# Optimization experiments

Hardware: AMD Instinct MI355X
Metric: run time of the kernel (lower is better)

Reference implementation:

```python
import jax, jax.numpy as jnp
import numpy as np

# Tree config: batch of perfect binary trees in heap layout (root=0, children of i are 2i+1, 2i+2)
D_MODEL = 512
DEPTH = 10                      # number of internal levels
B = 64                          # number of trees in the batch
VOCAB = 32000
N_LEAVES = 2 ** DEPTH           # 1024 leaves per tree
N_NODES = 2 ** (DEPTH + 1) - 1  # 2047 nodes per tree
N_CLASSES = 2                   # binary graph classification


def setup_inputs() -> dict:
    key = jax.random.key(0)
    k_tok, k_emb, k_iou, k_f, k_out = jax.random.split(key, 5)
    d = D_MODEL
    s_in = 1.0 / np.sqrt(2 * d)
    return {
        "tokens": jax.random.randint(k_tok, (B, N_LEAVES), 0, VOCAB, dtype=jnp.int32),
        "embedding": (jax.random.normal(k_emb, (VOCAB, d), jnp.float32) * 0.02),
        "W_iou": jax.random.normal(k_iou, (2 * d, 3 * d), jnp.float32) * s_in,
        "b_iou": jnp.zeros((3 * d,), jnp.float32),
        "W_f": jax.random.normal(k_f, (2 * d, 2 * d), jnp.float32) * s_in,
        "b_f": jnp.zeros((2 * d,), jnp.float32),
        "W_out": jax.random.normal(k_out, (d, N_CLASSES), jnp.float32) * (1.0 / np.sqrt(d)),
    }


def reference(tokens, embedding, W_iou, b_iou, W_f, b_f, W_out):
    # Shared activation / memory buffers over all nodes, as in RecursiveNN.forward.
    d = embedding.shape[1]
    b = tokens.shape[0]
    h = jnp.zeros((b, N_NODES, d), jnp.float32)   # activations
    c = jnp.zeros((b, N_NODES, d), jnp.float32)   # memory (memory_size=1)

    # Leaves: embedding lookup, scattered into the activation buffer.
    leaf_h = embedding[tokens]                    # [B, N_LEAVES, d]
    h = h.at[:, N_LEAVES - 1:].set(leaf_h)

    # Internal nodes by topological level (leaf-adjacent level first, root last).
    for level in range(DEPTH - 1, -1, -1):
        idx = np.arange(2 ** level - 1, 2 ** (level + 1) - 1)  # node group (static)
        left, right = 2 * idx + 1, 2 * idx + 2                 # predecessor indices
        # Gather predecessor activations and memory.
        hl, hr = h[:, left], h[:, right]                       # [B, n, d]
        cl, cr = c[:, left], c[:, right]
        x = jnp.concatenate([hl, hr], axis=-1)                 # [B, n, 2d]
        # Binary TreeLSTM cell (the _apply_function for the 'add' binary op).
        iou = x @ W_iou + b_iou
        i, o, u = jnp.split(iou, 3, axis=-1)
        f = jax.nn.sigmoid(x @ W_f + b_f)
        fl, fr = jnp.split(f, 2, axis=-1)
        c_new = jax.nn.sigmoid(i) * jnp.tanh(u) + fl * cl + fr * cr
        h_new = jax.nn.sigmoid(o) * jnp.tanh(c_new)
        # Scatter back into the shared buffers.
        h = h.at[:, idx].set(h_new)
        c = c.at[:, idx].set(c_new)

    # _compute_output: linear binary-classification head on the root activation.
    return h[:, 0] @ W_out                                     # [B, N_CLASSES]
```

## Files before the change

### kernel.cpp

```cpp
#include <hip/hip_runtime.h>
#include <math.h>

typedef unsigned short u16;
typedef short s16x8 __attribute__((ext_vector_type(8)));
typedef float f32x4 __attribute__((ext_vector_type(4)));

#define NITER 32
#define ARW 72

__device__ __align__(16) u16 g_Bhi[1024 * 2560];
__device__ __align__(16) u16 g_Blo[1024 * 2560];
__device__ __align__(16) u16 g_Aleaf[(size_t)64 * 1024 * 1024];

__device__ __forceinline__ u16 f2bf(float x) {
    unsigned u = __float_as_uint(x);
    u += 0x7fffu + ((u >> 16) & 1u);
    return (u16)(u >> 16);
}
__device__ __forceinline__ float bf2f(u16 h) { return __uint_as_float(((unsigned)h) << 16); }
__device__ __forceinline__ float sigm(float x) { return 1.0f / (1.0f + expf(-x)); }
__device__ __forceinline__ unsigned pk(u16 a, u16 b) { return (unsigned)a | ((unsigned)b << 16); }

__device__ __forceinline__ void gload16(const void* g, u16* l) {
    __builtin_amdgcn_global_load_lds(
        (const __attribute__((address_space(1))) void*)g,
        (__attribute__((address_space(3))) void*)(void*)l, 16, 0, 0);
}

__global__ __launch_bounds__(256)
void wsplit_kernel(const float* __restrict__ Wiou, const float* __restrict__ Wf)
{
    __shared__ float tile[32][65];
    const int kb = blockIdx.x;
    const int cb = blockIdx.y;
    const int t  = threadIdx.x;
    const int c0 = cb * 64;

    {
        const int kk  = t >> 3;
        const int cu0 = (t & 7) * 8;
        const int k   = kb * 32 + kk;
#pragma unroll
        for (int u = 0; u < 8; u++) {
            int c = c0 + cu0 + u;
            float v = (c < 1536) ? Wiou[(size_t)k * 1536 + c]
                                 : Wf[(size_t)k * 1024 + (c - 1536)];
            tile[kk][cu0 + u] = v;
        }
    }
    __syncthreads();
    {
        const int jl = t >> 2;
        const int kc = (t & 3) * 8;
        const int g  = c0 >> 9;
        const int j  = (c0 & 511) + jl;
        size_t dst = (((size_t)kb * 5 + g) * 512 + j) * 32 + kc;
        unsigned ph[4], pl[4];
#pragma unroll
        for (int u = 0; u < 4; u++) {
            float v0 = tile[kc + 2 * u][jl];
            float v1 = tile[kc + 2 * u + 1][jl];
            u16 h0 = f2bf(v0), h1 = f2bf(v1);
            u16 l0 = f2bf(v0 - bf2f(h0)), l1 = f2bf(v1 - bf2f(h1));
            ph[u] = pk(h0, h1);
            pl[u] = pk(l0, l1);
        }
        *(uint4*)(g_Bhi + dst) = make_uint4(ph[0], ph[1], ph[2], ph[3]);
        *(uint4*)(g_Blo + dst) = make_uint4(pl[0], pl[1], pl[2], pl[3]);
    }
}

__global__ __launch_bounds__(256)
void leafgather_kernel(const int* __restrict__ tokens, const float* __restrict__ emb)
{
    const int gidx = blockIdx.x * 256 + threadIdx.x;
    const int row  = gidx >> 5;
    const int c    = gidx & 31;
    const int tok  = tokens[row];
    const float* src = emb + (size_t)tok * 512 + c * 16;
    u16* dst = g_Aleaf + (size_t)row * 1024 + c * 32;

    float4 f0 = *(const float4*)(src);
    float4 f1 = *(const float4*)(src + 4);
    float4 f2 = *(const float4*)(src + 8);
    float4 f3 = *(const float4*)(src + 12);
    float v[16] = {f0.x,f0.y,f0.z,f0.w, f1.x,f1.y,f1.z,f1.w,
                   f2.x,f2.y,f2.z,f2.w, f3.x,f3.y,f3.z,f3.w};
    unsigned ph[8], pl[8];
#pragma unroll
    for (int i = 0; i < 8; i++) {
        u16 h0 = f2bf(v[2*i]),   h1 = f2bf(v[2*i+1]);
        u16 l0 = f2bf(v[2*i]   - bf2f(h0));
        u16 l1 = f2bf(v[2*i+1] - bf2f(h1));
        ph[i] = pk(h0, h1);
        pl[i] = pk(l0, l1);
    }
    *(uint4*)(dst)      = make_uint4(ph[0], ph[1], ph[2], ph[3]);
    *(uint4*)(dst + 8)  = make_uint4(ph[4], ph[5], ph[6], ph[7]);
    *(uint4*)(dst + 16) = make_uint4(pl[0], pl[1], pl[2], pl[3]);
    *(uint4*)(dst + 24) = make_uint4(pl[4], pl[5], pl[6], pl[7]);
}

template<bool LEAF>
__global__ __launch_bounds__(256, 2)
void level_big(const u16* __restrict__ Hcin, const float* __restrict__ Cc,
               const float* __restrict__ b_iou, const float* __restrict__ b_f,
               u16* __restrict__ Hp, float* __restrict__ Cp,
               int np, int lgnp)
{
    __shared__ __align__(16) u16 Ab0[8192];
    __shared__ __align__(16) u16 Ab1[8192];

    const u16* Hc = LEAF ? g_Aleaf : Hcin;

    const int tid = threadIdx.x;
    const int jg  = blockIdx.x;
    const int m0  = blockIdx.y * 64;
    const int j0  = jg * 64;
    const int nc  = np * 2;

    const int w    = tid >> 6;
    const int lane = tid & 63;
    const int il   = lane & 15;
    const int kq   = lane >> 4;
    const int wc   = w;

    f32x4 acc[4][5];
#pragma unroll
    for (int rf = 0; rf < 4; rf++)
#pragma unroll
        for (int g = 0; g < 5; g++) acc[rf][g] = (f32x4)0.0f;

    const int bA  = m0 >> lgnp;
    const int pA0 = m0 & (np - 1);
    const char* A0u = (const char*)(Hc + ((size_t)bA * nc + 2 * pA0) * 1024);
    const int rowS = tid >> 3;
    const int segS = (tid & 7) ^ (rowS & 7);
    const unsigned voffA = (unsigned)rowS * 4096u + (unsigned)segS * 16u;

    const int shi = ((kq >> 1) << 2) | (kq & 1);
    const int x7  = il & 7;
    const int aoh = il * 64 + ((shi ^ x7) * 8);
    const int aol = il * 64 + (((shi + 2) ^ x7) * 8);

    const char* BH0 = (const char*)(g_Bhi + (size_t)j0 * 32);
    const char* BL0 = (const char*)(g_Blo + (size_t)j0 * 32);
    unsigned vB[5];
#pragma unroll
    for (int g = 0; g < 5; g++)
        vB[g] = (unsigned)(((wc * 16 + il) * 32 + kq * 8) * 2 + g * 32768);

    s16x8 bh[5], bl[5];
    s16x8 ah[4], al[4];

#define STAGEA2(DST, t_)                                                       \
    {                                                                          \
        const char* ab = A0u + (size_t)(t_) * 128;                             \
        gload16(ab + voffA, (DST) + w * 512);                                  \
        gload16(ab + 131072 + voffA, (DST) + 2048 + w * 512);                  \
    }

#define LOADB_HI(t_)                                                           \
    {                                                                          \
        const char* bhp = BH0 + (size_t)(t_) * 163840;                         \
        _Pragma("unroll")                                                      \
        for (int g = 0; g < 5; g++) bh[g] = *(const s16x8*)(bhp + vB[g]);      \
    }

#define LOADB_LO(t_)                                                           \
    {                                                                          \
        const char* blp = BL0 + (size_t)(t_) * 163840;                         \
        _Pragma("unroll")                                                      \
        for (int g = 0; g < 5; g++) bl[g] = *(const s16x8*)(blp + vB[g]);      \
    }

#define READ_AH(ABASE)                                                         \
    {                                                                          \
        _Pragma("unroll")                                                      \
        for (int rf = 0; rf < 4; rf++)                                         \
            ah[rf] = *(const s16x8*)&(ABASE)[aoh + rf * 1024];                 \
    }

#define READ_AL(ABASE)                                                         \
    {                                                                          \
        _Pragma("unroll")                                                      \
        for (int rf = 0; rf < 4; rf++)                                         \
            al[rf] = *(const s16x8*)&(ABASE)[aol + rf * 1024];                 \
    }

#define MFMA_PASS(AREGS, BSET)                                                 \
    {                                                                          \
        __builtin_amdgcn_s_setprio(1);                                         \
        _Pragma("unroll")                                                      \
        for (int rf = 0; rf < 4; rf++)                                         \
            _Pragma("unroll")                                                  \
            for (int g = 0; g < 5; g++)                                        \
                acc[rf][g] = __builtin_amdgcn_mfma_f32_16x16x32_bf16(AREGS[rf], BSET[g], acc[rf][g], 0, 0, 0); \
        __builtin_amdgcn_s_setprio(0);                                         \
    }

#define WINDOW(ACUR, ANXT, t0_, more_)                                         \
    {                                                                          \
        if (more_) {                                                           \
            STAGEA2(ANXT, (t0_) + 2);                                          \
            STAGEA2((ANXT) + 4096, (t0_) + 3);                                 \
            __builtin_amdgcn_sched_barrier(0);                                 \
        }                                                                      \
                                    \
        MFMA_PASS(ah, bh);                                                     \
        MFMA_PASS(al, bh);                                \
        LOADB_HI((t0_) + 1);                                                   \
        READ_AL((ACUR) + 4096);                     \
        MFMA_PASS(ah, bl);                                \
        LOADB_LO((t0_) + 1);                                                   \
        READ_AH((ACUR) + 4096);                     \
                                         \
        MFMA_PASS(al, bh);                                                     \
        MFMA_PASS(ah, bh);                                        \
        if (more_) LOADB_HI((t0_) + 2);                                        \
        MFMA_PASS(ah, bl);                                        \
        if (more_) LOADB_LO((t0_) + 2);                                        \
        if (more_) {                                                           \
            asm volatile("s_waitcnt vmcnt(10)" ::: "memory");                  \
            __builtin_amdgcn_s_barrier();                                      \
            __builtin_amdgcn_sched_barrier(0);                                 \
            READ_AH(ANXT);                           \
            READ_AL(ANXT);                                                     \
        }                                                                      \
    }

    STAGEA2(Ab0, 0);
    STAGEA2(Ab0 + 4096, 1);
    __builtin_amdgcn_sched_barrier(0);
    LOADB_HI(0);
    LOADB_LO(0);
    asm volatile("s_waitcnt vmcnt(10)" ::: "memory");
    __builtin_amdgcn_s_barrier();
    __builtin_amdgcn_sched_barrier(0);
    READ_AH(Ab0);
    READ_AL(Ab0);

#pragma unroll 1
    for (int t0 = 0; t0 < NITER; t0 += 4) {
        WINDOW(Ab0, Ab1, t0, 1);
        WINDOW(Ab1, Ab0, t0 + 2, (t0 + 4 < NITER));
    }
#undef STAGEA2
#undef LOADB_HI
#undef LOADB_LO
#undef READ_AH
#undef READ_AL
#undef MFMA_PASS
#undef WINDOW

    const int jglob = j0 + wc * 16 + il;
    const float bi  = b_iou[jglob];
    const float bo_ = b_iou[512 + jglob];
    const float bu  = b_iou[1024 + jglob];
    const float bfl = b_f[jglob];
    const float bfr = b_f[512 + jglob];

#pragma unroll
    for (int rf = 0; rf < 4; rf++) {
#pragma unroll
        for (int r = 0; r < 4; r++) {
            const int m  = m0 + rf * 16 + kq * 4 + r;
            const int b  = m >> lgnp;
            const int p  = m & (np - 1);
            float i_ = acc[rf][0][r] + bi;
            float o_ = acc[rf][1][r] + bo_;
            float u_ = acc[rf][2][r] + bu;
            float fl = sigm(acc[rf][3][r] + bfl);
            float fr = sigm(acc[rf][4][r] + bfr);
            float cl = 0.0f, cr_ = 0.0f;
            if (!LEAF) {
                size_t cb_ = ((size_t)b * nc + 2 * p) * 512 + jglob;
                cl  = Cc[cb_];
                cr_ = Cc[cb_ + 512];
            }
            float cn = sigm(i_) * tanhf(u_) + fl * cl + fr * cr_;
            float hn = sigm(o_) * tanhf(cn);
            size_t prow = (size_t)b * np + p;
            u16 hh  = f2bf(hn);
            u16 hlo = f2bf(hn - bf2f(hh));
            Hp[prow * 1024 + (size_t)(jg * 4 + wc) * 32 + il]      = hh;
            Hp[prow * 1024 + (size_t)(jg * 4 + wc) * 32 + 16 + il] = hlo;
            Cp[prow * 512 + jglob] = cn;
        }
    }
}

__global__ __launch_bounds__(256, 2)
void level_small(const u16* __restrict__ Hc, const float* __restrict__ Cc,
                 const float* __restrict__ b_iou, const float* __restrict__ b_f,
                 u16* __restrict__ Hp, float* __restrict__ Cp,
                 int np, int lgnp)
{
    __shared__ __align__(16) u16 Ac[2][64 * ARW];

    const int tid = threadIdx.x;
    const int jg  = blockIdx.x;
    const int m0  = blockIdx.y * 64;
    const int j0  = jg * 64;
    const int nc  = np * 2;
    const int M   = np * 64;

    const int w    = tid >> 6;
    const int lane = tid & 63;
    const int il   = lane & 15;
    const int kq   = lane >> 4;
    const int wc   = w;

    f32x4 acc[4][5];
#pragma unroll
    for (int rf = 0; rf < 4; rf++)
#pragma unroll
        for (int g = 0; g < 5; g++) acc[rf][g] = (f32x4)0.0f;

    const int rA = tid >> 2;
    const int qA = tid & 3;
    int mA = m0 + rA; if (mA > M - 1) mA = M - 1;
    const int bA = mA >> lgnp;
    const int pA = mA & (np - 1);
    const u16* arow = Hc + ((size_t)bA * nc + 2 * pA) * 1024;
    const int daI = rA * ARW + (qA & 1) * 32 + (qA >> 1) * 16;

    const char* BH0 = (const char*)(g_Bhi + (size_t)j0 * 32);
    const char* BL0 = (const char*)(g_Blo + (size_t)j0 * 32);
    unsigned vB[5];
#pragma unroll
    for (int g = 0; g < 5; g++)
        vB[g] = (unsigned)(((wc * 16 + il) * 32 + kq * 8) * 2 + g * 32768);

    uint4  aR0, aR1;
    s16x8 b0h[5], b0l[5], b1h[5], b1l[5];

#define LOADA(t_)                                                              \
    {                                                                          \
        const u16* asrc = arow + (t_) * 64 + qA * 16;                          \
        aR0 = *(const uint4*)asrc;                                             \
        aR1 = *(const uint4*)(asrc + 8);                                       \
    }
#define LOADB(BH, BL, t_)                                                      \
    {                                                                          \
        const char* bh = BH0 + (size_t)(t_) * 163840;                          \
        const char* bl = BL0 + (size_t)(t_) * 163840;                          \
        _Pragma("unroll")                                                      \
        for (int g = 0; g < 5; g++) {                                          \
            BH[g] = *(const s16x8*)(bh + vB[g]);                               \
            BL[g] = *(const s16x8*)(bl + vB[g]);                               \
        }                                                                      \
    }
#define WRITEA(bf)                                                             \
    {                                                                          \
        *(uint4*)&Ac[bf][daI]     = aR0;                                       \
        *(uint4*)&Ac[bf][daI + 8] = aR1;                                       \
    }
#define COMPUTE(BH, BL, BUF)                                                   \
    {                                                                          \
        _Pragma("unroll")                                                      \
        for (int rf = 0; rf < 4; rf++) {                                       \
            const int ao = (rf * 16 + il) * ARW + kq * 8;                      \
            s16x8 ahv = *(const s16x8*)&Ac[BUF][ao];                           \
            s16x8 alv = *(const s16x8*)&Ac[BUF][ao + 32];                      \
            _Pragma("unroll")                                                  \
            for (int g = 0; g < 5; g++) {                                      \
                acc[rf][g] = __builtin_amdgcn_mfma_f32_16x16x32_bf16(ahv, BH[g], acc[rf][g], 0, 0, 0); \
                acc[rf][g] = __builtin_amdgcn_mfma_f32_16x16x32_bf16(ahv, BL[g], acc[rf][g], 0, 0, 0); \
                acc[rf][g] = __builtin_amdgcn_mfma_f32_16x16x32_bf16(alv, BH[g], acc[rf][g], 0, 0, 0); \
            }                                                                  \
        }                                                                      \
    }

    LOADA(0);
    LOADB(b0h, b0l, 0);
    WRITEA(0);
    __syncthreads();

#pragma unroll 1
    for (int t = 0; t < NITER; t += 2) {
        if (t + 1 < NITER) { LOADA(t + 1); LOADB(b1h, b1l, t + 1); }
        COMPUTE(b0h, b0l, 0);
        if (t + 1 < NITER) { WRITEA(1); __syncthreads(); }
        if (t + 2 < NITER) { LOADA(t + 2); LOADB(b0h, b0l, t + 2); }
        COMPUTE(b1h, b1l, 1);
        if (t + 2 < NITER) { WRITEA(0); __syncthreads(); }
    }
#undef LOADA
#undef LOADB
#undef WRITEA
#undef COMPUTE

    const int jglob = j0 + wc * 16 + il;
    const float bi  = b_iou[jglob];
    const float bo_ = b_iou[512 + jglob];
    const float bu  = b_iou[1024 + jglob];
    const float bfl = b_f[jglob];
    const float bfr = b_f[512 + jglob];

#pragma unroll
    for (int rf = 0; rf < 4; rf++) {
#pragma unroll
        for (int r = 0; r < 4; r++) {
            const int m = m0 + rf * 16 + kq * 4 + r;
            if (m < M) {
                const int b = m >> lgnp;
                const int p = m & (np - 1);
                float i_ = acc[rf][0][r] + bi;
                float o_ = acc[rf][1][r] + bo_;
                float u_ = acc[rf][2][r] + bu;
                float fl = sigm(acc[rf][3][r] + bfl);
                float fr = sigm(acc[rf][4][r] + bfr);
                size_t cb_ = ((size_t)b * nc + 2 * p) * 512 + jglob;
                float cl  = Cc[cb_];
                float cr_ = Cc[cb_ + 512];
                float cn = sigm(i_) * tanhf(u_) + fl * cl + fr * cr_;
                float hn = sigm(o_) * tanhf(cn);
                size_t prow = (size_t)b * np + p;
                u16 hh  = f2bf(hn);
                u16 hlo = f2bf(hn - bf2f(hh));
                Hp[prow * 1024 + (size_t)(jg * 4 + wc) * 32 + il]      = hh;
                Hp[prow * 1024 + (size_t)(jg * 4 + wc) * 32 + 16 + il] = hlo;
                Cp[prow * 512 + jglob] = cn;
            }
        }
    }
}

__global__ __launch_bounds__(256)
void out_kernel(const u16* __restrict__ Hroot, const float* __restrict__ W_out,
                float* __restrict__ out)
{
    const int b = blockIdx.x;
    const int tid = threadIdx.x;
    float s0 = 0.f, s1 = 0.f;
    for (int d = tid; d < 512; d += 256) {
        const u16* row = Hroot + (size_t)b * 1024 + (d >> 4) * 32 + (d & 15);
        float h = bf2f(row[0]) + bf2f(row[16]);
        s0 = fmaf(h, W_out[d * 2 + 0], s0);
        s1 = fmaf(h, W_out[d * 2 + 1], s1);
    }
#pragma unroll
    for (int off = 32; off > 0; off >>= 1) {
        s0 += __shfl_down(s0, off, 64);
        s1 += __shfl_down(s1, off, 64);
    }
    __shared__ float red[2][4];
    const int wave = tid >> 6;
    if ((tid & 63) == 0) { red[0][wave] = s0; red[1][wave] = s1; }
    __syncthreads();
    if (tid == 0) {
        float t0 = 0.f, t1 = 0.f;
#pragma unroll
        for (int wv = 0; wv < 4; wv++) { t0 += red[0][wv]; t1 += red[1][wv]; }
        out[b * 2 + 0] = t0;
        out[b * 2 + 1] = t1;
    }
}

extern "C" void kernel_launch(void* const* d_in, const int* in_sizes, int n_in,
                              void* d_out, int out_size, void* d_ws, size_t ws_size,
                              hipStream_t stream)
{
    const int*   tokens = (const int*)  d_in[0];
    const float* emb    = (const float*)d_in[1];
    const float* W_iou  = (const float*)d_in[2];
    const float* b_iou  = (const float*)d_in[3];
    const float* W_f    = (const float*)d_in[4];
    const float* b_f    = (const float*)d_in[5];
    const float* W_out  = (const float*)d_in[6];
    float* out = (float*)d_out;

    u16*   H0 = (u16*)d_ws;
    float* C0 = (float*)(H0 + (size_t)512 * 64 * 1024);
    u16*   H1 = (u16*)(C0 + (size_t)512 * 64 * 512);
    float* C1 = (float*)(H1 + (size_t)256 * 64 * 1024);

    wsplit_kernel<<<dim3(32, 40), 256, 0, stream>>>(W_iou, W_f);
    leafgather_kernel<<<8192, 256, 0, stream>>>(tokens, emb);

    level_big<true><<<dim3(8, 512), 256, 0, stream>>>(
        nullptr, nullptr, b_iou, b_f, H0, C0, 512, 9);

    u16* Hc = H0;  float* Cc = C0;
    u16* Hp = H1;  float* Cp = C1;
    for (int L = 8; L >= 0; L--) {
        const int np = 1 << L;
        if (np >= 64) {
            level_big<false><<<dim3(8, np), 256, 0, stream>>>(
                Hc, Cc, b_iou, b_f, Hp, Cp, np, L);
        } else {
            level_small<<<dim3(8, np), 256, 0, stream>>>(
                Hc, Cc, b_iou, b_f, Hp, Cp, np, L);
        }
        u16* tH = Hc; Hc = Hp; Hp = tH;
        float* tC = Cc; Cc = Cp; Cp = tC;
    }

    out_kernel<<<64, 256, 0, stream>>>(Hc, W_out, out);
}
```

Before: 1.233 ms.

## Rewrite small-level kernel with narrower column tiles and async LDS pipeline

The small-level kernel (levels with fewer than 64 parents per tree) now gives each block 16 output columns instead of 64, so it launches 4x more blocks on the low-occupancy upper levels. It reuses the big kernel's global_load_lds staging, swizzled LDS layout and software-pipelined MFMA window in place of register-staged A tiles. Each wave now handles its own 16 rows with one accumulator set, and the m<M guard is gone. The cost is that each block reloads the B weights for fewer columns, raising weight traffic per useful FLOP.

```diff
diff --git a/kernel.cpp b/kernel.cpp
--- a/kernel.cpp
+++ b/kernel.cpp
@@ -6,7 +6,6 @@
 typedef float f32x4 __attribute__((ext_vector_type(4)));
 
 #define NITER 32
-#define ARW 72
 
 __device__ __align__(16) u16 g_Bhi[1024 * 2560];
 __device__ __align__(16) u16 g_Blo[1024 * 2560];
@@ -206,25 +205,23 @@
             STAGEA2((ANXT) + 4096, (t0_) + 3);                                 \
             __builtin_amdgcn_sched_barrier(0);                                 \
         }                                                                      \
-                                    \
         MFMA_PASS(ah, bh);                                                     \
-        MFMA_PASS(al, bh);                                \
+        MFMA_PASS(al, bh);                                                     \
         LOADB_HI((t0_) + 1);                                                   \
-        READ_AL((ACUR) + 4096);                     \
-        MFMA_PASS(ah, bl);                                \
+        READ_AL((ACUR) + 4096);                                                \
+        MFMA_PASS(ah, bl);                                                     \
         LOADB_LO((t0_) + 1);                                                   \
-        READ_AH((ACUR) + 4096);                     \
-                                         \
+        READ_AH((ACUR) + 4096);                                                \
         MFMA_PASS(al, bh);                                                     \
-        MFMA_PASS(ah, bh);                                        \
+        MFMA_PASS(ah, bh);                                                     \
         if (more_) LOADB_HI((t0_) + 2);                                        \
-        MFMA_PASS(ah, bl);                                        \
+        MFMA_PASS(ah, bl);                                                     \
         if (more_) LOADB_LO((t0_) + 2);                                        \
         if (more_) {                                                           \
             asm volatile("s_waitcnt vmcnt(10)" ::: "memory");                  \
             __builtin_amdgcn_s_barrier();                                      \
             __builtin_amdgcn_sched_barrier(0);                                 \
-            READ_AH(ANXT);                           \
+            READ_AH(ANXT);                                                     \
             READ_AL(ANXT);                                                     \
         }                                                                      \
     }
@@ -291,107 +288,133 @@
 }
 
 __global__ __launch_bounds__(256, 2)
-void level_small(const u16* __restrict__ Hc, const float* __restrict__ Cc,
-                 const float* __restrict__ b_iou, const float* __restrict__ b_f,
-                 u16* __restrict__ Hp, float* __restrict__ Cp,
-                 int np, int lgnp)
+void level_small2(const u16* __restrict__ Hc, const float* __restrict__ Cc,
+                  const float* __restrict__ b_iou, const float* __restrict__ b_f,
+                  u16* __restrict__ Hp, float* __restrict__ Cp,
+                  int np, int lgnp)
 {
-    __shared__ __align__(16) u16 Ac[2][64 * ARW];
+    __shared__ __align__(16) u16 Ab0[8192];
+    __shared__ __align__(16) u16 Ab1[8192];
 
     const int tid = threadIdx.x;
     const int jg  = blockIdx.x;
     const int m0  = blockIdx.y * 64;
-    const int j0  = jg * 64;
+    const int j0  = jg * 16;
     const int nc  = np * 2;
-    const int M   = np * 64;
 
     const int w    = tid >> 6;
     const int lane = tid & 63;
     const int il   = lane & 15;
     const int kq   = lane >> 4;
-    const int wc   = w;
-
-    f32x4 acc[4][5];
-#pragma unroll
-    for (int rf = 0; rf < 4; rf++)
-#pragma unroll
-        for (int g = 0; g < 5; g++) acc[rf][g] = (f32x4)0.0f;
-
-    const int rA = tid >> 2;
-    const int qA = tid & 3;
-    int mA = m0 + rA; if (mA > M - 1) mA = M - 1;
-    const int bA = mA >> lgnp;
-    const int pA = mA & (np - 1);
-    const u16* arow = Hc + ((size_t)bA * nc + 2 * pA) * 1024;
-    const int daI = rA * ARW + (qA & 1) * 32 + (qA >> 1) * 16;
+
+    f32x4 acc[5];
+#pragma unroll
+    for (int g = 0; g < 5; g++) acc[g] = (f32x4)0.0f;
+
+    const char* A0u = (const char*)(Hc + (size_t)m0 * 2048);
+    const int rowS = tid >> 3;
+    const int segS = (tid & 7) ^ (rowS & 7);
+    const unsigned voffA = (unsigned)rowS * 4096u + (unsigned)segS * 16u;
+
+    const int shi = ((kq >> 1) << 2) | (kq & 1);
+    const int x7  = il & 7;
+    const int aoh = (w * 16 + il) * 64 + ((shi ^ x7) * 8);
+    const int aol = (w * 16 + il) * 64 + (((shi + 2) ^ x7) * 8);
 
     const char* BH0 = (const char*)(g_Bhi + (size_t)j0 * 32);
     const char* BL0 = (const char*)(g_Blo + (size_t)j0 * 32);
     unsigned vB[5];
 #pragma unroll
     for (int g = 0; g < 5; g++)
-        vB[g] = (unsigned)(((wc * 16 + il) * 32 + kq * 8) * 2 + g * 32768);
-
-    uint4  aR0, aR1;
-    s16x8 b0h[5], b0l[5], b1h[5], b1l[5];
-
-#define LOADA(t_)                                                              \
-    {                                                                          \
-        const u16* asrc = arow + (t_) * 64 + qA * 16;                          \
-        aR0 = *(const uint4*)asrc;                                             \
-        aR1 = *(const uint4*)(asrc + 8);                                       \
-    }
-#define LOADB(BH, BL, t_)                                                      \
-    {                                                                          \
-        const char* bh = BH0 + (size_t)(t_) * 163840;                          \
-        const char* bl = BL0 + (size_t)(t_) * 163840;                          \
-        _Pragma("unroll")                                                      \
-        for (int g = 0; g < 5; g++) {                                          \
-            BH[g] = *(const s16x8*)(bh + vB[g]);                               \
-            BL[g] = *(const s16x8*)(bl + vB[g]);                               \
+        vB[g] = (unsigned)((il * 32 + kq * 8) * 2 + g * 32768);
+
+    s16x8 bh[5], bl[5];
+    s16x8 ah, al;
+
+#define SSTAGEA2(DST, t_)                                                      \
+    {                                                                          \
+        const char* ab = A0u + (size_t)(t_) * 128;                             \
+        gload16(ab + voffA, (DST) + w * 512);                                  \
+        gload16(ab + 131072 + voffA, (DST) + 2048 + w * 512);                  \
+    }
+
+#define SLOADB_HI(t_)                                                          \
+    {                                                                          \
+        const char* bhp = BH0 + (size_t)(t_) * 163840;                         \
+        _Pragma("unroll")                                                      \
+        for (int g = 0; g < 5; g++) bh[g] = *(const s16x8*)(bhp + vB[g]);      \
+    }
+
+#define SLOADB_LO(t_)                                                          \
+    {                                                                          \
+        const char* blp = BL0 + (size_t)(t_) * 163840;                         \
+        _Pragma("unroll")                                                      \
+        for (int g = 0; g < 5; g++) bl[g] = *(const s16x8*)(blp + vB[g]);      \
+    }
+
+#define SREAD_AH(ABASE)  { ah = *(const s16x8*)&(ABASE)[aoh]; }
+#define SREAD_AL(ABASE)  { al = *(const s16x8*)&(ABASE)[aol]; }
+
+#define SMFMA_PASS(AREG, BSET)                                                 \
+    {                                                                          \
+        _Pragma("unroll")                                                      \
+        for (int g = 0; g < 5; g++)                                            \
+            acc[g] = __builtin_amdgcn_mfma_f32_16x16x32_bf16(AREG, BSET[g], acc[g], 0, 0, 0); \
+    }
+
+#define SWINDOW(ACUR, ANXT, t0_, more_)                                        \
+    {                                                                          \
+        if (more_) {                                                           \
+            SSTAGEA2(ANXT, (t0_) + 2);                                         \
+            SSTAGEA2((ANXT) + 4096, (t0_) + 3);                                \
+            __builtin_amdgcn_sched_barrier(0);                                 \
         }                                                                      \
-    }
-#define WRITEA(bf)                                                             \
-    {                                                                          \
-        *(uint4*)&Ac[bf][daI]     = aR0;                                       \
-        *(uint4*)&Ac[bf][daI + 8] = aR1;                                       \
-    }
-#define COMPUTE(BH, BL, BUF)                                                   \
-    {                                                                          \
-        _Pragma("unroll")                                                      \
-        for (int rf = 0; rf < 4; rf++) {                                       \
-            const int ao = (rf * 16 + il) * ARW + kq * 8;                      \
-            s16x8 ahv = *(const s16x8*)&Ac[BUF][ao];                           \
-            s16x8 alv = *(const s16x8*)&Ac[BUF][ao + 32];                      \
-            _Pragma("unroll")                                                  \
-            for (int g = 0; g < 5; g++) {                                      \
-                acc[rf][g] = __builtin_amdgcn_mfma_f32_16x16x32_bf16(ahv, BH[g], acc[rf][g], 0, 0, 0); \
-                acc[rf][g] = __builtin_amdgcn_mfma_f32_16x16x32_bf16(ahv, BL[g], acc[rf][g], 0, 0, 0); \
-                acc[rf][g] = __builtin_amdgcn_mfma_f32_16x16x32_bf16(alv, BH[g], acc[rf][g], 0, 0, 0); \
-            }                                                                  \
+        SMFMA_PASS(ah, bh);                                                    \
+        SMFMA_PASS(al, bh);                                                    \
+        SLOADB_HI((t0_) + 1);                                                  \
+        SREAD_AL((ACUR) + 4096);                                               \
+        SMFMA_PASS(ah, bl);                                                    \
+        SLOADB_LO((t0_) + 1);                                                  \
+        SREAD_AH((ACUR) + 4096);                                               \
+        SMFMA_PASS(al, bh);                                                    \
+        SMFMA_PASS(ah, bh);                                                    \
+        if (more_) SLOADB_HI((t0_) + 2);                                       \
+        SMFMA_PASS(ah, bl);                                                    \
+        if (more_) SLOADB_LO((t0_) + 2);                                       \
+        if (more_) {                                                           \
+            asm volatile("s_waitcnt vmcnt(10)" ::: "memory");                  \
+            __builtin_amdgcn_s_barrier();                                      \
+            __builtin_amdgcn_sched_barrier(0);                                 \
+            SREAD_AH(ANXT);                                                    \
+            SREAD_AL(ANXT);                                                    \
         }                                                                      \
     }
 
-    LOADA(0);
-    LOADB(b0h, b0l, 0);
-    WRITEA(0);
-    __syncthreads();
+    SSTAGEA2(Ab0, 0);
+    SSTAGEA2(Ab0 + 4096, 1);
+    __builtin_amdgcn_sched_barrier(0);
+    SLOADB_HI(0);
+    SLOADB_LO(0);
+    asm volatile("s_waitcnt vmcnt(10)" ::: "memory");
+    __builtin_amdgcn_s_barrier();
+    __builtin_amdgcn_sched_barrier(0);
+    SREAD_AH(Ab0);
+    SREAD_AL(Ab0);
 
 #pragma unroll 1
-    for (int t = 0; t < NITER; t += 2) {
-        if (t + 1 < NITER) { LOADA(t + 1); LOADB(b1h, b1l, t + 1); }
-        COMPUTE(b0h, b0l, 0);
-        if (t + 1 < NITER) { WRITEA(1); __syncthreads(); }
-        if (t + 2 < NITER) { LOADA(t + 2); LOADB(b0h, b0l, t + 2); }
-        COMPUTE(b1h, b1l, 1);
-        if (t + 2 < NITER) { WRITEA(0); __syncthreads(); }
-    }
-#undef LOADA
-#undef LOADB
-#undef WRITEA
-#undef COMPUTE
-
-    const int jglob = j0 + wc * 16 + il;
+    for (int t0 = 0; t0 < NITER; t0 += 4) {
+        SWINDOW(Ab0, Ab1, t0, 1);
+        SWINDOW(Ab1, Ab0, t0 + 2, (t0 + 4 < NITER));
+    }
+#undef SSTAGEA2
+#undef SLOADB_HI
+#undef SLOADB_LO
+#undef SREAD_AH
+#undef SREAD_AL
+#undef SMFMA_PASS
+#undef SWINDOW
+
+    const int jglob = j0 + il;
     const float bi  = b_iou[jglob];
     const float bo_ = b_iou[512 + jglob];
     const float bu  = b_iou[1024 + jglob];
@@ -399,31 +422,26 @@
     const float bfr = b_f[512 + jglob];
 
 #pragma unroll
-    for (int rf = 0; rf < 4; rf++) {
-#pragma unroll
-        for (int r = 0; r < 4; r++) {
-            const int m = m0 + rf * 16 + kq * 4 + r;
-            if (m < M) {
-                const int b = m >> lgnp;
-                const int p = m & (np - 1);
-                float i_ = acc[rf][0][r] + bi;
-                float o_ = acc[rf][1][r] + bo_;
-                float u_ = acc[rf][2][r] + bu;
-                float fl = sigm(acc[rf][3][r] + bfl);
-                float fr = sigm(acc[rf][4][r] + bfr);
-                size_t cb_ = ((size_t)b * nc + 2 * p) * 512 + jglob;
-                float cl  = Cc[cb_];
-                float cr_ = Cc[cb_ + 512];
-                float cn = sigm(i_) * tanhf(u_) + fl * cl + fr * cr_;
-                float hn = sigm(o_) * tanhf(cn);
-                size_t prow = (size_t)b * np + p;
-                u16 hh  = f2bf(hn);
-                u16 hlo = f2bf(hn - bf2f(hh));
-                Hp[prow * 1024 + (size_t)(jg * 4 + wc) * 32 + il]      = hh;
-                Hp[prow * 1024 + (size_t)(jg * 4 + wc) * 32 + 16 + il] = hlo;
-                Cp[prow * 512 + jglob] = cn;
-            }
-        }
+    for (int r = 0; r < 4; r++) {
+        const int m = m0 + w * 16 + kq * 4 + r;
+        const int b = m >> lgnp;
+        const int p = m & (np - 1);
+        float i_ = acc[0][r] + bi;
+        float o_ = acc[1][r] + bo_;
+        float u_ = acc[2][r] + bu;
+        float fl = sigm(acc[3][r] + bfl);
+        float fr = sigm(acc[4][r] + bfr);
+        size_t cb_ = ((size_t)b * nc + 2 * p) * 512 + jglob;
+        float cl  = Cc[cb_];
+        float cr_ = Cc[cb_ + 512];
+        float cn = sigm(i_) * tanhf(u_) + fl * cl + fr * cr_;
+        float hn = sigm(o_) * tanhf(cn);
+        size_t prow = (size_t)b * np + p;
+        u16 hh  = f2bf(hn);
+        u16 hlo = f2bf(hn - bf2f(hh));
+        Hp[prow * 1024 + (size_t)jg * 32 + il]      = hh;
+        Hp[prow * 1024 + (size_t)jg * 32 + 16 + il] = hlo;
+        Cp[prow * 512 + jglob] = cn;
     }
 }
 
@@ -490,7 +508,7 @@
             level_big<false><<<dim3(8, np), 256, 0, stream>>>(
                 Hc, Cc, b_iou, b_f, Hp, Cp, np, L);
         } else {
-            level_small<<<dim3(8, np), 256, 0, stream>>>(
+            level_small2<<<dim3(32, np), 256, 0, stream>>>(
                 Hc, Cc, b_iou, b_f, Hp, Cp, np, L);
         }
         u16* tH = Hc; Hc = Hp; Hp = tH;
```

Result: faster. 1.175 ms (median of 2 runs) (-4.7%).
